# Kernel tuning notes

Measured on AMD Instinct MI355X. Metric: run time of the kernel, lower is better.

The kernel has to match this reference:

```python
import jax, jax.numpy as jnp
import numpy as np

T, D, N, K, H, F = 2048, 4096, 32, 8, 128, 14336
THETA = 500000.0
EPS = 1e-5


def setup_inputs() -> dict:
    key = jax.random.key(0)
    ks = jax.random.split(key, 10)
    s = 0.02  # weight init scale
    return {
        "x": jax.random.normal(ks[0], (T, D), jnp.float32),
        "positions": jnp.arange(T, dtype=jnp.int32),
        "ln1_scale": jnp.ones((D,), jnp.float32),
        "w_q": jax.random.normal(ks[1], (D, N, H), jnp.float32) * s,
        "w_k": jax.random.normal(ks[2], (D, K, H), jnp.float32) * s,
        "w_v": jax.random.normal(ks[3], (D, K, H), jnp.float32) * s,
        "w_o": jax.random.normal(ks[4], (N, H, D), jnp.float32) * s,
        "ln2_scale": jnp.ones((D,), jnp.float32),
        "w_gate": jax.random.normal(ks[5], (D, F), jnp.float32) * s,
        "w_up": jax.random.normal(ks[6], (D, F), jnp.float32) * s,
        "w_down": jax.random.normal(ks[7], (F, D), jnp.float32) * s,
    }


def _rms_norm(x, scale):
    var = jnp.mean(jnp.square(x), axis=-1, keepdims=True)
    return x * jax.lax.rsqrt(var + EPS) * scale


def _apply_rope(x, pos):
    # x: [T, heads, H]; Llama rotate-half RoPE
    half = H // 2
    inv_freq = 1.0 / (THETA ** (jnp.arange(half, dtype=jnp.float32) / half))
    ang = pos.astype(jnp.float32)[:, None] * inv_freq[None, :]      # [T, half]
    cos = jnp.cos(ang)[:, None, :]
    sin = jnp.sin(ang)[:, None, :]
    x1, x2 = x[..., :half], x[..., half:]
    return jnp.concatenate([x1 * cos - x2 * sin, x2 * cos + x1 * sin], axis=-1)


def reference(x, positions, ln1_scale, w_q, w_k, w_v, w_o, ln2_scale, w_gate, w_up, w_down):
    # --- input RMSNorm ---
    h = _rms_norm(x, ln1_scale)
    # --- QKV projections + RoPE ---
    q = _apply_rope(jnp.einsum('td,dnh->tnh', h, w_q), positions)   # [T,N,H]
    k = _apply_rope(jnp.einsum('td,dkh->tkh', h, w_k), positions)   # [T,K,H]
    v = jnp.einsum('td,dkh->tkh', h, w_v)                            # [T,K,H]
    # --- GQA causal attention (prefill) ---
    G = N // K
    qg = q.reshape(T, K, G, H)
    scale = 1.0 / jnp.sqrt(jnp.float32(H))
    scores = jnp.einsum('tkgh,skh->kgts', qg, k) * scale             # [K,G,T,T]
    causal = positions[:, None] >= positions[None, :]                # [T,T]
    scores = jnp.where(causal[None, None], scores, jnp.finfo(scores.dtype).min)
    probs = jax.nn.softmax(scores, axis=-1)
    attn = jnp.einsum('kgts,skh->tkgh', probs, v).reshape(T, N, H)
    attn_out = jnp.einsum('tnh,nhd->td', attn, w_o)
    # --- residual ---
    residual = attn_out + x
    # --- post-attn RMSNorm + SwiGLU MLP ---
    h2 = _rms_norm(residual, ln2_scale)
    gate = jax.nn.silu(h2 @ w_gate)
    up = h2 @ w_up
    out = (gate * up) @ w_down
    return residual + out
```

## Files before the change

### kernel.cpp

```cpp
#include <hip/hip_runtime.h>

typedef __attribute__((ext_vector_type(8))) short bf16x8;
typedef __attribute__((ext_vector_type(4))) float f32x4;

constexpr int T = 2048;
constexpr int D = 4096;
constexpr int NQ = 32;
constexpr int NKV = 8;
constexpr int H = 128;
constexpr int F = 14336;
constexpr int NQKV = (NQ + 2 * NKV) * H;
constexpr int VOFF = (NQ + NKV) * H;

__device__ inline unsigned short f2bf(float f) {
  unsigned u = __float_as_uint(f);
  return (unsigned short)((u + 0x7FFFu + ((u >> 16) & 1u)) >> 16);
}

__device__ inline void gload_lds16(const void* g, void* l) {
  __builtin_amdgcn_global_load_lds((const __attribute__((address_space(1))) void*)g,
                                   (__attribute__((address_space(3))) void*)l, 16, 0, 0);
}

#define MFMA16(a, b, c) __builtin_amdgcn_mfma_f32_16x16x32_bf16(a, b, c, 0, 0, 0)

template <int MODE>
__global__ __launch_bounds__(256) void transpose_bf16(const float* __restrict__ in,
                                                      unsigned short* __restrict__ out,
                                                      int K, int N) {
  __shared__ float tile[64 * 65];
  const int kb = blockIdx.x * 64;
  const int nb = blockIdx.y * 64;
  const int tid = threadIdx.x;
  const int r = tid >> 2;
  const int c4 = tid & 3;
#pragma unroll
  for (int i = 0; i < 4; ++i) {
    float4 v = *(const float4*)(in + (size_t)(kb + r) * N + nb + c4 * 16 + i * 4);
    *(float4*)&tile[r * 65 + c4 * 16 + i * 4] = v;
  }
  __syncthreads();
  const int n = tid >> 2;
  const int kq = tid & 3;
  int nsrc = nb + n;
  int prow = (MODE == 0) ? nsrc : ((nsrc >> 4) * 32 + (nsrc & 15) + (MODE == 2 ? 16 : 0));
#pragma unroll
  for (int half = 0; half < 2; ++half) {
    ushort4 o0, o1;
    int k0 = kq * 16 + half * 8;
    o0.x = f2bf(tile[(k0 + 0) * 65 + n]);
    o0.y = f2bf(tile[(k0 + 1) * 65 + n]);
    o0.z = f2bf(tile[(k0 + 2) * 65 + n]);
    o0.w = f2bf(tile[(k0 + 3) * 65 + n]);
    o1.x = f2bf(tile[(k0 + 4) * 65 + n]);
    o1.y = f2bf(tile[(k0 + 5) * 65 + n]);
    o1.z = f2bf(tile[(k0 + 6) * 65 + n]);
    o1.w = f2bf(tile[(k0 + 7) * 65 + n]);
    unsigned short* op = out + (size_t)prow * K + kb + k0;
    *(ushort4*)(op + 0) = o0;
    *(ushort4*)(op + 4) = o1;
  }
}

__global__ __launch_bounds__(256) void rmsnorm_kernel(
    const float* __restrict__ in, const float* __restrict__ scale,
    unsigned short* __restrict__ out) {
  int row = blockIdx.x;
  const float4* xr = (const float4*)(in + (size_t)row * D);
  const float4* sr = (const float4*)scale;
  float4 vals[4];
  float ss = 0.f;
#pragma unroll
  for (int i = 0; i < 4; ++i) {
    float4 v = xr[threadIdx.x + i * 256];
    vals[i] = v;
    ss += v.x * v.x + v.y * v.y + v.z * v.z + v.w * v.w;
  }
#pragma unroll
  for (int off = 32; off; off >>= 1) ss += __shfl_xor(ss, off, 64);
  __shared__ float wsum[4];
  if ((threadIdx.x & 63) == 0) wsum[threadIdx.x >> 6] = ss;
  __syncthreads();
  float r = rsqrtf((wsum[0] + wsum[1] + wsum[2] + wsum[3]) * (1.f / D) + 1e-5f);
#pragma unroll
  for (int i = 0; i < 4; ++i) {
    int vi = threadIdx.x + i * 256;
    float4 v = vals[i];
    float4 s = sr[vi];
    ushort4 o;
    o.x = f2bf(v.x * r * s.x);
    o.y = f2bf(v.y * r * s.y);
    o.z = f2bf(v.z * r * s.z);
    o.w = f2bf(v.w * r * s.w);
    *(ushort4*)(out + (size_t)row * D + (size_t)vi * 4) = o;
  }
}

__global__ __launch_bounds__(256) void add3_kernel(const float* __restrict__ a,
                                                   const float* __restrict__ b,
                                                   const float* __restrict__ c,
                                                   float* __restrict__ o) {
  int i = blockIdx.x * 256 + threadIdx.x;
  float4 va = ((const float4*)a)[i];
  float4 vb = ((const float4*)b)[i];
  float4 vc = ((const float4*)c)[i];
  float4 vo;
  vo.x = va.x + vb.x + vc.x;
  vo.y = va.y + vb.y + vc.y;
  vo.z = va.z + vb.z + vc.z;
  vo.w = va.w + vb.w + vc.w;
  ((float4*)o)[i] = vo;
}

__global__ __launch_bounds__(256) void rope_table(const int* __restrict__ pos,
                                                  float* __restrict__ ctab,
                                                  float* __restrict__ stab) {
  int idx = blockIdx.x * 256 + threadIdx.x;
  int t = idx >> 6, i = idx & 63;
  float inv = exp2f(-(float)i * (log2f(500000.0f) / 64.0f));
  float ang = (float)pos[t] * inv;
  ctab[idx] = cosf(ang);
  stab[idx] = sinf(ang);
}

__global__ __launch_bounds__(256) void rope_bf16(const float* __restrict__ x,
                                                 const float* __restrict__ ctab,
                                                 const float* __restrict__ stab,
                                                 unsigned short* __restrict__ out,
                                                 int nheads, int row_stride, float scale) {
  int idx = blockIdx.x * 256 + threadIdx.x;
  int i = idx & 63;
  int tn = idx >> 6;
  int t = tn / nheads;
  int n = tn - t * nheads;
  float c = ctab[t * 64 + i], s = stab[t * 64 + i];
  const float* p = x + (size_t)t * row_stride + n * H;
  float x1 = p[i], x2 = p[i + 64];
  unsigned short* o = out + (size_t)tn * H;
  o[i] = f2bf((x1 * c - x2 * s) * scale);
  o[i + 64] = f2bf((x2 * c + x1 * s) * scale);
}

template <int EP>
__global__ __launch_bounds__(256) void gemm_bf(
    const unsigned short* __restrict__ A, const unsigned short* __restrict__ Bt0,
    float* __restrict__ outF, unsigned short* __restrict__ outB, int Kd, int Nd) {
  __shared__ unsigned short lA[128 * 32];
  __shared__ unsigned short lB0[128 * 32];

  const int tid = threadIdx.x;
  const int m0 = blockIdx.x * 128;
  const int n0 = blockIdx.y * 128;
  const int lane = tid & 63;
  const int wv = tid >> 6;

  f32x4 acc[4][4];
#pragma unroll
  for (int i = 0; i < 4; ++i)
#pragma unroll
    for (int j = 0; j < 4; ++j) acc[i][j] = (f32x4){0.f, 0.f, 0.f, 0.f};

  const int wr = (wv >> 1) * 64;
  const int wc = (wv & 1) * 64;
  const int k8 = (lane >> 4) * 8;
  const int rl = lane & 15;
  const int sidx0 = wv * 512 + lane * 8;

  for (int k0 = 0; k0 < Kd; k0 += 32) {
    __syncthreads();
#pragma unroll
    for (int it = 0; it < 2; ++it) {
      int idx = sidx0 + it * 2048;
      int row = idx >> 5, kk = idx & 31;
      int base = wv * 512 + it * 2048;
      gload_lds16(A + (size_t)(m0 + row) * Kd + k0 + kk, &lA[base]);
      gload_lds16(Bt0 + (size_t)(n0 + row) * Kd + k0 + kk, &lB0[base]);
    }
    asm volatile("s_waitcnt vmcnt(0)" ::: "memory");
    __syncthreads();

    bf16x8 af[4], bfr[4];
#pragma unroll
    for (int i = 0; i < 4; ++i)
      af[i] = *(const bf16x8*)&lA[(wr + i * 16 + rl) * 32 + k8];
#pragma unroll
    for (int j = 0; j < 4; ++j)
      bfr[j] = *(const bf16x8*)&lB0[(wc + j * 16 + rl) * 32 + k8];
#pragma unroll
    for (int i = 0; i < 4; ++i)
#pragma unroll
      for (int j = 0; j < 4; ++j)
        acc[i][j] = MFMA16(af[i], bfr[j], acc[i][j]);
  }

  const int rb = (lane >> 4) * 4;
#pragma unroll
  for (int i = 0; i < 4; ++i)
#pragma unroll
    for (int j = 0; j < 4; ++j) {
      int col = n0 + wc + j * 16 + rl;
      if (EP == 4 && n0 >= VOFF) {
        int row0 = m0 + wr + i * 16 + rb;
        ushort4 o;
        o.x = f2bf(acc[i][j][0]);
        o.y = f2bf(acc[i][j][1]);
        o.z = f2bf(acc[i][j][2]);
        o.w = f2bf(acc[i][j][3]);
        *(ushort4*)&outB[(size_t)(col - VOFF) * T + row0] = o;
      } else {
#pragma unroll
        for (int jj = 0; jj < 4; ++jj) {
          int row = m0 + wr + i * 16 + rb + jj;
          outF[(size_t)row * Nd + col] = acc[i][j][jj];
        }
      }
    }
}

template <int EP>
__global__ __launch_bounds__(512, 2) void gemm256(
    const unsigned short* __restrict__ A, const unsigned short* __restrict__ Bt,
    float* __restrict__ outF, float* __restrict__ outF2,
    unsigned short* __restrict__ outB, int Kd, int Nd, int Klen) {
  __shared__ unsigned short lds[65536];
  const int tid = threadIdx.x, lane = tid & 63, wv = tid >> 6;
  const int wm = wv >> 2, wn = wv & 3;
  const int rl = lane & 15, g = lane >> 4;
  const int kz = blockIdx.z;
  int raw = blockIdx.x + blockIdx.y * gridDim.x;
  int cpx = (gridDim.x * gridDim.y) >> 3;
  int sid = (raw & 7) * cpx + (raw >> 3);
  int brow = sid % gridDim.x;
  int bcol = sid / gridDim.x;
  const int m0 = brow * 256, n0 = bcol * 256;

  const int l8 = lane >> 3;
  const int scol = ((lane & 7) ^ l8) * 8;
  const int xr = (rl & 7) << 4;
  const int pc0 = (g * 16) ^ xr;
  const int pc1 = (64 + g * 16) ^ xr;

  const char* ldsc = (const char*)lds;
  const unsigned short* gA = A + (size_t)(m0 + wv * 8 + l8) * Kd + kz * Klen + scol;
  const unsigned short* gB = Bt + (size_t)(n0 + wv * 8 + l8) * Kd + kz * Klen + scol;

  f32x4 acc[8][4];
#pragma unroll
  for (int i = 0; i < 8; ++i)
#pragma unroll
    for (int j = 0; j < 4; ++j) acc[i][j] = (f32x4){0.f, 0.f, 0.f, 0.f};

  const int NT = Klen >> 6;

#define STAGE_AL(kt, l)                                                      \
  gload_lds16(gA + (size_t)(kt) * 64 + (size_t)(l) * 64 * Kd,                \
              (void*)&lds[((kt) & 1) * 32768 + (l) * 4096 + wv * 512]);
#define STAGE_BL(kt, l)                                                      \
  gload_lds16(gB + (size_t)(kt) * 64 + (size_t)(l) * 64 * Kd,                \
              (void*)&lds[((kt) & 1) * 32768 + 16384 + (l) * 4096 + wv * 512]);
#define SBAR()                        \
  __builtin_amdgcn_sched_barrier(0);  \
  __builtin_amdgcn_s_barrier();

  STAGE_AL(0, 0); STAGE_AL(0, 1); STAGE_AL(0, 2); STAGE_AL(0, 3);
  STAGE_BL(0, 0); STAGE_BL(0, 1); STAGE_BL(0, 2); STAGE_BL(0, 3);
  STAGE_AL(1, 0); STAGE_AL(1, 1); STAGE_AL(1, 2); STAGE_AL(1, 3);
  STAGE_BL(1, 0); STAGE_BL(1, 1); STAGE_BL(1, 2); STAGE_BL(1, 3);
  asm volatile("s_waitcnt vmcnt(8)" ::: "memory");
  SBAR();

  const int bhalf = (wn >> 1) * 16384;
  const int brl = (wn & 1) * 64;

  for (int kt = 0; kt < NT; ++kt) {
    const int b = kt & 1;
    const char* aB = ldsc + b * 65536 + wm * 16384;
    const char* bB = ldsc + b * 65536 + 32768 + bhalf;
    const bool pre = (kt + 2 < NT);
    bf16x8 aLo[4][2], aHi[4][2], bLo[2][2], bHi[2][2];
#pragma unroll
    for (int mf = 0; mf < 4; ++mf) {
      aLo[mf][0] = *(const bf16x8*)(aB + (mf * 16 + rl) * 128 + pc0);
      aLo[mf][1] = *(const bf16x8*)(aB + (mf * 16 + rl) * 128 + pc1);
    }
#pragma unroll
    for (int nf = 0; nf < 2; ++nf) {
      bLo[nf][0] = *(const bf16x8*)(bB + (brl + nf * 16 + rl) * 128 + pc0);
      bLo[nf][1] = *(const bf16x8*)(bB + (brl + nf * 16 + rl) * 128 + pc1);
    }
    SBAR();
    __builtin_amdgcn_s_setprio(1);
#pragma unroll
    for (int mf = 0; mf < 4; ++mf)
#pragma unroll
      for (int nf = 0; nf < 2; ++nf) {
        acc[mf][nf] = MFMA16(aLo[mf][0], bLo[nf][0], acc[mf][nf]);
        acc[mf][nf] = MFMA16(aLo[mf][1], bLo[nf][1], acc[mf][nf]);
      }
    __builtin_amdgcn_s_setprio(0);
    SBAR();
#pragma unroll
    for (int nf = 0; nf < 2; ++nf) {
      bHi[nf][0] = *(const bf16x8*)(bB + (brl + (nf + 2) * 16 + rl) * 128 + pc0);
      bHi[nf][1] = *(const bf16x8*)(bB + (brl + (nf + 2) * 16 + rl) * 128 + pc1);
    }
    if (pre) { STAGE_AL(kt + 2, 0); STAGE_AL(kt + 2, 2); }
    SBAR();
    __builtin_amdgcn_s_setprio(1);
#pragma unroll
    for (int mf = 0; mf < 4; ++mf)
#pragma unroll
      for (int nf = 0; nf < 2; ++nf) {
        acc[mf][nf + 2] = MFMA16(aLo[mf][0], bHi[nf][0], acc[mf][nf + 2]);
        acc[mf][nf + 2] = MFMA16(aLo[mf][1], bHi[nf][1], acc[mf][nf + 2]);
      }
    __builtin_amdgcn_s_setprio(0);
    SBAR();
#pragma unroll
    for (int mf = 0; mf < 4; ++mf) {
      aHi[mf][0] = *(const bf16x8*)(aB + ((mf + 4) * 16 + rl) * 128 + pc0);
      aHi[mf][1] = *(const bf16x8*)(aB + ((mf + 4) * 16 + rl) * 128 + pc1);
    }
    if (pre) { STAGE_BL(kt + 2, 0); STAGE_BL(kt + 2, 1); }
    SBAR();
    __builtin_amdgcn_s_setprio(1);
#pragma unroll
    for (int mf = 0; mf < 4; ++mf)
#pragma unroll
      for (int nf = 0; nf < 2; ++nf) {
        acc[mf + 4][nf + 2] = MFMA16(aHi[mf][0], bHi[nf][0], acc[mf + 4][nf + 2]);
        acc[mf + 4][nf + 2] = MFMA16(aHi[mf][1], bHi[nf][1], acc[mf + 4][nf + 2]);
      }
    __builtin_amdgcn_s_setprio(0);
    SBAR();
    if (pre) {
      STAGE_BL(kt + 2, 2); STAGE_BL(kt + 2, 3);
      STAGE_AL(kt + 2, 1); STAGE_AL(kt + 2, 3);
    }
    __builtin_amdgcn_s_setprio(1);
#pragma unroll
    for (int mf = 0; mf < 4; ++mf)
#pragma unroll
      for (int nf = 0; nf < 2; ++nf) {
        acc[mf + 4][nf] = MFMA16(aHi[mf][0], bLo[nf][0], acc[mf + 4][nf]);
        acc[mf + 4][nf] = MFMA16(aHi[mf][1], bLo[nf][1], acc[mf + 4][nf]);
      }
    __builtin_amdgcn_s_setprio(0);
    if (pre) {
      asm volatile("s_waitcnt vmcnt(8)" ::: "memory");
    } else if (kt + 1 < NT) {
      asm volatile("s_waitcnt vmcnt(0)" ::: "memory");
    }
    SBAR();
  }

  const int g4 = g * 4;
  if constexpr (EP == 5) {
    const int acolBase = ((n0 + wn * 64) >> 1) + rl;
#pragma unroll
    for (int mf = 0; mf < 8; ++mf)
#pragma unroll
      for (int p = 0; p < 2; ++p) {
        int acol = acolBase + p * 16;
#pragma unroll
        for (int jj = 0; jj < 4; ++jj) {
          int row = m0 + wm * 128 + mf * 16 + g4 + jj;
          float gg = acc[mf][2 * p][jj];
          float uu = acc[mf][2 * p + 1][jj];
          outB[(size_t)row * F + acol] = f2bf(gg / (1.f + __expf(-gg)) * uu);
        }
      }
  } else {
    float* dst = kz ? outF2 : outF;
#pragma unroll
    for (int mf = 0; mf < 8; ++mf)
#pragma unroll
      for (int q = 0; q < 4; ++q) {
        int col = n0 + wn * 64 + q * 16 + rl;
#pragma unroll
        for (int jj = 0; jj < 4; ++jj) {
          int row = m0 + wm * 128 + mf * 16 + g4 + jj;
          dst[(size_t)row * Nd + col] = acc[mf][q][jj];
        }
      }
  }
#undef STAGE_AL
#undef STAGE_BL
#undef SBAR
}

constexpr int KLD = 136;
constexpr int VLD = 72;
constexpr int PLD = 72;

__global__ __launch_bounds__(256) void flash_attn(
    const unsigned short* __restrict__ qbf, const unsigned short* __restrict__ kbf,
    const unsigned short* __restrict__ vtbf, unsigned short* __restrict__ out) {
  __shared__ unsigned short K_lds[64 * KLD];
  __shared__ unsigned short Vt_lds[H * VLD];
  __shared__ unsigned short P_lds[4 * 16 * PLD];

  const int tid = threadIdx.x;
  const int lane = tid & 63;
  const int wave = tid >> 6;
  const int qb = blockIdx.x;
  const int n = blockIdx.y;
  const int kvh = n >> 2;
  const int g = lane >> 4;
  const int rl = lane & 15;
  const int qrow = qb * 64 + wave * 16;

  bf16x8 qfrag[4];
  {
    const unsigned short* qp = qbf + ((size_t)(qrow + rl) * NQ + n) * H + g * 8;
#pragma unroll
    for (int ks = 0; ks < 4; ++ks) qfrag[ks] = *(const bf16x8*)(qp + ks * 32);
  }

  f32x4 oacc[8];
#pragma unroll
  for (int ob = 0; ob < 8; ++ob) oacc[ob] = (f32x4){0.f, 0.f, 0.f, 0.f};
  float mrun[4] = {-1e30f, -1e30f, -1e30f, -1e30f};
  float lrun[4] = {0.f, 0.f, 0.f, 0.f};

  const int krow = tid >> 2, kseg = (tid & 3) * 32;
  const int vh = tid >> 1, vseg = (tid & 1) * 32;

  for (int kt = 0; kt <= qb; ++kt) {
    const int kbase = kt * 64;
    __syncthreads();
    {
      const unsigned short* kp = kbf + ((size_t)(kbase + krow) * NKV + kvh) * H + kseg;
#pragma unroll
      for (int i = 0; i < 4; ++i)
        *(bf16x8*)&K_lds[krow * KLD + kseg + i * 8] = *(const bf16x8*)(kp + i * 8);
      const unsigned short* vp = vtbf + (size_t)(kvh * H + vh) * T + kbase + vseg;
#pragma unroll
      for (int i = 0; i < 4; ++i)
        *(bf16x8*)&Vt_lds[vh * VLD + vseg + i * 8] = *(const bf16x8*)(vp + i * 8);
    }
    __syncthreads();

    f32x4 sacc[4];
#pragma unroll
    for (int cb = 0; cb < 4; ++cb) sacc[cb] = (f32x4){0.f, 0.f, 0.f, 0.f};
#pragma unroll
    for (int cb = 0; cb < 4; ++cb)
#pragma unroll
      for (int ks = 0; ks < 4; ++ks) {
        bf16x8 kf = *(const bf16x8*)&K_lds[(cb * 16 + rl) * KLD + ks * 32 + g * 8];
        sacc[cb] = MFMA16(qfrag[ks], kf, sacc[cb]);
      }

    if (kt == qb) {
#pragma unroll
      for (int cb = 0; cb < 4; ++cb) {
        int kvg = cb * 16 + rl;
#pragma unroll
        for (int r = 0; r < 4; ++r) {
          int qrel = wave * 16 + g * 4 + r;
          if (kvg > qrel) sacc[cb][r] = -1e30f;
        }
      }
    }

    float mx[4], sm[4], corr[4];
#pragma unroll
    for (int r = 0; r < 4; ++r) {
      float m0 = fmaxf(fmaxf(sacc[0][r], sacc[1][r]), fmaxf(sacc[2][r], sacc[3][r]));
#pragma unroll
      for (int off = 1; off < 16; off <<= 1) m0 = fmaxf(m0, __shfl_xor(m0, off, 64));
      float nm = fmaxf(mrun[r], m0);
      corr[r] = __expf(mrun[r] - nm);
      mrun[r] = nm;
      mx[r] = nm;
    }
#pragma unroll
    for (int cb = 0; cb < 4; ++cb)
#pragma unroll
      for (int r = 0; r < 4; ++r) sacc[cb][r] = __expf(sacc[cb][r] - mx[r]);
#pragma unroll
    for (int r = 0; r < 4; ++r) {
      float s0 = sacc[0][r] + sacc[1][r] + sacc[2][r] + sacc[3][r];
#pragma unroll
      for (int off = 1; off < 16; off <<= 1) s0 += __shfl_xor(s0, off, 64);
      sm[r] = s0;
      lrun[r] = lrun[r] * corr[r] + sm[r];
    }
#pragma unroll
    for (int ob = 0; ob < 8; ++ob)
#pragma unroll
      for (int r = 0; r < 4; ++r) oacc[ob][r] *= corr[r];

#pragma unroll
    for (int cb = 0; cb < 4; ++cb)
#pragma unroll
      for (int r = 0; r < 4; ++r)
        P_lds[(wave * 16 + g * 4 + r) * PLD + cb * 16 + rl] = f2bf(sacc[cb][r]);

    bf16x8 pa[2];
#pragma unroll
    for (int ks = 0; ks < 2; ++ks)
      pa[ks] = *(const bf16x8*)&P_lds[(wave * 16 + rl) * PLD + ks * 32 + g * 8];

#pragma unroll
    for (int ob = 0; ob < 8; ++ob)
#pragma unroll
      for (int ks = 0; ks < 2; ++ks) {
        bf16x8 vf = *(const bf16x8*)&Vt_lds[(ob * 16 + rl) * VLD + ks * 32 + g * 8];
        oacc[ob] = MFMA16(pa[ks], vf, oacc[ob]);
      }
  }

  float inv[4];
#pragma unroll
  for (int r = 0; r < 4; ++r) inv[r] = 1.f / lrun[r];
#pragma unroll
  for (int ob = 0; ob < 8; ++ob)
#pragma unroll
    for (int r = 0; r < 4; ++r) {
      int t = qrow + g * 4 + r;
      out[((size_t)t * NQ + n) * H + ob * 16 + rl] = f2bf(oacc[ob][r] * inv[r]);
    }
}

extern "C" void kernel_launch(void* const* d_in, const int* in_sizes, int n_in,
                              void* d_out, int out_size, void* d_ws, size_t ws_size,
                              hipStream_t stream) {
  (void)in_sizes; (void)n_in; (void)out_size; (void)ws_size;
  const float* x = (const float*)d_in[0];
  const int* positions = (const int*)d_in[1];
  const float* ln1 = (const float*)d_in[2];
  const float* w_q = (const float*)d_in[3];
  const float* w_k = (const float*)d_in[4];
  const float* w_v = (const float*)d_in[5];
  const float* w_o = (const float*)d_in[6];
  const float* ln2 = (const float*)d_in[7];
  const float* w_gate = (const float*)d_in[8];
  const float* w_up = (const float*)d_in[9];
  const float* w_down = (const float*)d_in[10];
  float* out = (float*)d_out;

  char* ws = (char*)d_ws;
  size_t off = 0;
  auto alloc = [&](size_t bytes) {
    char* p = ws + off;
    off += (bytes + 255) & ~(size_t)255;
    return p;
  };
  unsigned short* h_bf = (unsigned short*)alloc((size_t)T * D * 2);
  unsigned short* h2_bf = (unsigned short*)alloc((size_t)T * D * 2);
  unsigned short* attn_bf = (unsigned short*)alloc((size_t)T * NQ * H * 2);
  unsigned short* act_bf = (unsigned short*)alloc((size_t)T * F * 2);
  float* qkvf = (float*)alloc((size_t)T * NQKV * 4);
  float* resid = (float*)alloc((size_t)T * D * 4);
  float* ctab = (float*)alloc((size_t)T * 64 * 4);
  float* stab = (float*)alloc((size_t)T * 64 * 4);
  unsigned short* qbf = (unsigned short*)alloc((size_t)T * NQ * H * 2);
  unsigned short* kbf = (unsigned short*)alloc((size_t)T * NKV * H * 2);
  unsigned short* vtbf = (unsigned short*)alloc((size_t)NKV * H * T * 2);
  unsigned short* wqkvt = (unsigned short*)alloc((size_t)NQKV * D * 2);
  unsigned short* wot = (unsigned short*)alloc((size_t)D * NQ * H * 2);
  unsigned short* wgut = (unsigned short*)alloc((size_t)2 * F * D * 2);
  unsigned short* wdt = (unsigned short*)alloc((size_t)D * F * 2);
  float* part0 = qkvf;
  float* part1 = (float*)wqkvt;

  transpose_bf16<0><<<dim3(D / 64, (NQ * H) / 64), 256, 0, stream>>>(w_q, wqkvt, D, NQ * H);
  transpose_bf16<0><<<dim3(D / 64, (NKV * H) / 64), 256, 0, stream>>>(
      w_k, wqkvt + (size_t)NQ * H * D, D, NKV * H);
  transpose_bf16<0><<<dim3(D / 64, (NKV * H) / 64), 256, 0, stream>>>(
      w_v, wqkvt + (size_t)VOFF * D, D, NKV * H);
  transpose_bf16<0><<<dim3((NQ * H) / 64, D / 64), 256, 0, stream>>>(w_o, wot, NQ * H, D);
  transpose_bf16<1><<<dim3(D / 64, F / 64), 256, 0, stream>>>(w_gate, wgut, D, F);
  transpose_bf16<2><<<dim3(D / 64, F / 64), 256, 0, stream>>>(w_up, wgut, D, F);
  transpose_bf16<0><<<dim3(F / 64, D / 64), 256, 0, stream>>>(w_down, wdt, F, D);

  rmsnorm_kernel<<<T, 256, 0, stream>>>(x, ln1, h_bf);
  rope_table<<<(T * 64) / 256, 256, 0, stream>>>(positions, ctab, stab);
  gemm_bf<4><<<dim3(T / 128, NQKV / 128), 256, 0, stream>>>(
      h_bf, wqkvt, qkvf, vtbf, D, NQKV);
  rope_bf16<<<(T * NQ * 64) / 256, 256, 0, stream>>>(qkvf, ctab, stab, qbf, NQ, NQKV,
                                                     0.08838834764831845f);
  rope_bf16<<<(T * NKV * 64) / 256, 256, 0, stream>>>(qkvf + NQ * H, ctab, stab, kbf,
                                                      NKV, NQKV, 1.0f);
  flash_attn<<<dim3(T / 64, NQ), 256, 0, stream>>>(qbf, kbf, vtbf, attn_bf);
  gemm256<0><<<dim3(T / 256, D / 256, 2), 512, 0, stream>>>(
      attn_bf, wot, part0, part1, nullptr, NQ * H, D, NQ * H / 2);
  add3_kernel<<<(T * D / 4) / 256, 256, 0, stream>>>(part0, part1, x, resid);
  rmsnorm_kernel<<<T, 256, 0, stream>>>(resid, ln2, h2_bf);
  gemm256<5><<<dim3(T / 256, (2 * F) / 256), 512, 0, stream>>>(
      h2_bf, wgut, nullptr, nullptr, act_bf, D, 2 * F, D);
  gemm256<0><<<dim3(T / 256, D / 256, 2), 512, 0, stream>>>(
      act_bf, wdt, part0, part1, nullptr, F, D, F / 2);
  add3_kernel<<<(T * D / 4) / 256, 256, 0, stream>>>(part0, part1, resid, out);
}
```

Measured before the change: 1.401 ms.

## Fuse residual add into RMSNorm, share KV tiles across GQA heads, prefetch B fragments

Three separate changes land together. First, the split-K partial sum plus residual add is fused into the second RMSNorm, which removes one full read and write pass over the residual. Second, flash attention now runs 512 threads per block covering all four query heads of a KV group over 32 query rows, so each K/V tile is loaded once per group instead of once per query head. Third, the 256-tile GEMM main loop reorders its B-tile staging and waits so that the next iteration's B low fragments are read from LDS early and carried in registers. The GEMM change raises register pressure and shifts the vmcnt wait points, and the attention change alters grid size and occupancy.

Result: no change. 1.378 ms (-1.6%).

```diff
diff --git a/kernel.cpp b/kernel.cpp
--- a/kernel.cpp
+++ b/kernel.cpp
@@ -86,6 +86,51 @@
   for (int i = 0; i < 4; ++i) {
     int vi = threadIdx.x + i * 256;
     float4 v = vals[i];
+    float4 s = sr[vi];
+    ushort4 o;
+    o.x = f2bf(v.x * r * s.x);
+    o.y = f2bf(v.y * r * s.y);
+    o.z = f2bf(v.z * r * s.z);
+    o.w = f2bf(v.w * r * s.w);
+    *(ushort4*)(out + (size_t)row * D + (size_t)vi * 4) = o;
+  }
+}
+
+__global__ __launch_bounds__(256) void rmsnorm_add3(
+    const float* __restrict__ a, const float* __restrict__ b,
+    const float* __restrict__ c, const float* __restrict__ scale,
+    float* __restrict__ residOut, unsigned short* __restrict__ out) {
+  int row = blockIdx.x;
+  const float4* ar = (const float4*)(a + (size_t)row * D);
+  const float4* br = (const float4*)(b + (size_t)row * D);
+  const float4* cr = (const float4*)(c + (size_t)row * D);
+  const float4* sr = (const float4*)scale;
+  float4* rr = (float4*)(residOut + (size_t)row * D);
+  float4 vals[4];
+  float ss = 0.f;
+#pragma unroll
+  for (int i = 0; i < 4; ++i) {
+    int vi = threadIdx.x + i * 256;
+    float4 va = ar[vi], vb = br[vi], vc = cr[vi];
+    float4 v;
+    v.x = va.x + vb.x + vc.x;
+    v.y = va.y + vb.y + vc.y;
+    v.z = va.z + vb.z + vc.z;
+    v.w = va.w + vb.w + vc.w;
+    vals[i] = v;
+    ss += v.x * v.x + v.y * v.y + v.z * v.z + v.w * v.w;
+  }
+#pragma unroll
+  for (int off = 32; off; off >>= 1) ss += __shfl_xor(ss, off, 64);
+  __shared__ float wsum[4];
+  if ((threadIdx.x & 63) == 0) wsum[threadIdx.x >> 6] = ss;
+  __syncthreads();
+  float r = rsqrtf((wsum[0] + wsum[1] + wsum[2] + wsum[3]) * (1.f / D) + 1e-5f);
+#pragma unroll
+  for (int i = 0; i < 4; ++i) {
+    int vi = threadIdx.x + i * 256;
+    float4 v = vals[i];
+    rr[vi] = v;
     float4 s = sr[vi];
     ushort4 o;
     o.x = f2bf(v.x * r * s.x);
@@ -272,30 +317,36 @@
   const int bhalf = (wn >> 1) * 16384;
   const int brl = (wn & 1) * 64;
 
+  bf16x8 bLoC[2][2];
+  {
+    const char* bB0 = ldsc + 32768 + bhalf;
+#pragma unroll
+    for (int nf = 0; nf < 2; ++nf) {
+      bLoC[nf][0] = *(const bf16x8*)(bB0 + (brl + nf * 16 + rl) * 128 + pc0);
+      bLoC[nf][1] = *(const bf16x8*)(bB0 + (brl + nf * 16 + rl) * 128 + pc1);
+    }
+  }
+
   for (int kt = 0; kt < NT; ++kt) {
     const int b = kt & 1;
     const char* aB = ldsc + b * 65536 + wm * 16384;
     const char* bB = ldsc + b * 65536 + 32768 + bhalf;
+    const char* bBn = ldsc + (b ^ 1) * 65536 + 32768 + bhalf;
     const bool pre = (kt + 2 < NT);
-    bf16x8 aLo[4][2], aHi[4][2], bLo[2][2], bHi[2][2];
+    bf16x8 aLo[4][2], aHi[4][2], bHi[2][2], bLoN[2][2];
 #pragma unroll
     for (int mf = 0; mf < 4; ++mf) {
       aLo[mf][0] = *(const bf16x8*)(aB + (mf * 16 + rl) * 128 + pc0);
       aLo[mf][1] = *(const bf16x8*)(aB + (mf * 16 + rl) * 128 + pc1);
     }
-#pragma unroll
-    for (int nf = 0; nf < 2; ++nf) {
-      bLo[nf][0] = *(const bf16x8*)(bB + (brl + nf * 16 + rl) * 128 + pc0);
-      bLo[nf][1] = *(const bf16x8*)(bB + (brl + nf * 16 + rl) * 128 + pc1);
-    }
     SBAR();
     __builtin_amdgcn_s_setprio(1);
 #pragma unroll
     for (int mf = 0; mf < 4; ++mf)
 #pragma unroll
       for (int nf = 0; nf < 2; ++nf) {
-        acc[mf][nf] = MFMA16(aLo[mf][0], bLo[nf][0], acc[mf][nf]);
-        acc[mf][nf] = MFMA16(aLo[mf][1], bLo[nf][1], acc[mf][nf]);
+        acc[mf][nf] = MFMA16(aLo[mf][0], bLoC[nf][0], acc[mf][nf]);
+        acc[mf][nf] = MFMA16(aLo[mf][1], bLoC[nf][1], acc[mf][nf]);
       }
     __builtin_amdgcn_s_setprio(0);
     SBAR();
@@ -321,7 +372,13 @@
       aHi[mf][0] = *(const bf16x8*)(aB + ((mf + 4) * 16 + rl) * 128 + pc0);
       aHi[mf][1] = *(const bf16x8*)(aB + ((mf + 4) * 16 + rl) * 128 + pc1);
     }
-    if (pre) { STAGE_BL(kt + 2, 0); STAGE_BL(kt + 2, 1); }
+    if (pre) {
+      STAGE_BL(kt + 2, 0); STAGE_BL(kt + 2, 1);
+      STAGE_BL(kt + 2, 2); STAGE_BL(kt + 2, 3);
+      asm volatile("s_waitcnt vmcnt(6)" ::: "memory");
+    } else {
+      asm volatile("s_waitcnt vmcnt(0)" ::: "memory");
+    }
     SBAR();
     __builtin_amdgcn_s_setprio(1);
 #pragma unroll
@@ -333,25 +390,32 @@
       }
     __builtin_amdgcn_s_setprio(0);
     SBAR();
-    if (pre) {
-      STAGE_BL(kt + 2, 2); STAGE_BL(kt + 2, 3);
-      STAGE_AL(kt + 2, 1); STAGE_AL(kt + 2, 3);
-    }
+    if (pre) { STAGE_AL(kt + 2, 1); STAGE_AL(kt + 2, 3); }
+    if (kt + 1 < NT) {
+#pragma unroll
+      for (int nf = 0; nf < 2; ++nf) {
+        bLoN[nf][0] = *(const bf16x8*)(bBn + (brl + nf * 16 + rl) * 128 + pc0);
+        bLoN[nf][1] = *(const bf16x8*)(bBn + (brl + nf * 16 + rl) * 128 + pc1);
+      }
+    }
+    SBAR();
     __builtin_amdgcn_s_setprio(1);
 #pragma unroll
     for (int mf = 0; mf < 4; ++mf)
 #pragma unroll
       for (int nf = 0; nf < 2; ++nf) {
-        acc[mf + 4][nf] = MFMA16(aHi[mf][0], bLo[nf][0], acc[mf + 4][nf]);
-        acc[mf + 4][nf] = MFMA16(aHi[mf][1], bLo[nf][1], acc[mf + 4][nf]);
+        acc[mf + 4][nf] = MFMA16(aHi[mf][0], bLoC[nf][0], acc[mf + 4][nf]);
+        acc[mf + 4][nf] = MFMA16(aHi[mf][1], bLoC[nf][1], acc[mf + 4][nf]);
       }
     __builtin_amdgcn_s_setprio(0);
-    if (pre) {
-      asm volatile("s_waitcnt vmcnt(8)" ::: "memory");
-    } else if (kt + 1 < NT) {
-      asm volatile("s_waitcnt vmcnt(0)" ::: "memory");
-    }
-    SBAR();
+    SBAR();
+    if (kt + 1 < NT) {
+#pragma unroll
+      for (int nf = 0; nf < 2; ++nf) {
+        bLoC[nf][0] = bLoN[nf][0];
+        bLoC[nf][1] = bLoN[nf][1];
+      }
+    }
   }
 
   const int g4 = g * 4;
@@ -393,22 +457,23 @@
 constexpr int VLD = 72;
 constexpr int PLD = 72;
 
-__global__ __launch_bounds__(256) void flash_attn(
+__global__ __launch_bounds__(512) void flash_attn(
     const unsigned short* __restrict__ qbf, const unsigned short* __restrict__ kbf,
     const unsigned short* __restrict__ vtbf, unsigned short* __restrict__ out) {
   __shared__ unsigned short K_lds[64 * KLD];
   __shared__ unsigned short Vt_lds[H * VLD];
-  __shared__ unsigned short P_lds[4 * 16 * PLD];
+  __shared__ unsigned short P_lds[8 * 16 * PLD];
 
   const int tid = threadIdx.x;
   const int lane = tid & 63;
-  const int wave = tid >> 6;
+  const int wv = tid >> 6;
   const int qb = blockIdx.x;
-  const int n = blockIdx.y;
-  const int kvh = n >> 2;
+  const int kvh = blockIdx.y;
+  const int qh = wv & 3, rh = wv >> 2;
+  const int n = kvh * 4 + qh;
   const int g = lane >> 4;
   const int rl = lane & 15;
-  const int qrow = qb * 64 + wave * 16;
+  const int qrow = qb * 32 + rh * 16;
 
   bf16x8 qfrag[4];
   {
@@ -423,21 +488,20 @@
   float mrun[4] = {-1e30f, -1e30f, -1e30f, -1e30f};
   float lrun[4] = {0.f, 0.f, 0.f, 0.f};
 
-  const int krow = tid >> 2, kseg = (tid & 3) * 32;
-  const int vh = tid >> 1, vseg = (tid & 1) * 32;
-
-  for (int kt = 0; kt <= qb; ++kt) {
+  const int krow = tid >> 3, kseg = (tid & 7) * 16;
+  const int vh = tid >> 2, vseg = (tid & 3) * 16;
+
+  const int ktmax = (qb * 32 + 31) >> 6;
+  for (int kt = 0; kt <= ktmax; ++kt) {
     const int kbase = kt * 64;
     __syncthreads();
     {
       const unsigned short* kp = kbf + ((size_t)(kbase + krow) * NKV + kvh) * H + kseg;
-#pragma unroll
-      for (int i = 0; i < 4; ++i)
-        *(bf16x8*)&K_lds[krow * KLD + kseg + i * 8] = *(const bf16x8*)(kp + i * 8);
+      *(bf16x8*)&K_lds[krow * KLD + kseg] = *(const bf16x8*)kp;
+      *(bf16x8*)&K_lds[krow * KLD + kseg + 8] = *(const bf16x8*)(kp + 8);
       const unsigned short* vp = vtbf + (size_t)(kvh * H + vh) * T + kbase + vseg;
-#pragma unroll
-      for (int i = 0; i < 4; ++i)
-        *(bf16x8*)&Vt_lds[vh * VLD + vseg + i * 8] = *(const bf16x8*)(vp + i * 8);
+      *(bf16x8*)&Vt_lds[vh * VLD + vseg] = *(const bf16x8*)vp;
+      *(bf16x8*)&Vt_lds[vh * VLD + vseg + 8] = *(const bf16x8*)(vp + 8);
     }
     __syncthreads();
 
@@ -452,14 +516,13 @@
         sacc[cb] = MFMA16(qfrag[ks], kf, sacc[cb]);
       }
 
-    if (kt == qb) {
+    if (kt == ktmax) {
 #pragma unroll
       for (int cb = 0; cb < 4; ++cb) {
-        int kvg = cb * 16 + rl;
+        int kv_abs = kbase + cb * 16 + rl;
 #pragma unroll
         for (int r = 0; r < 4; ++r) {
-          int qrel = wave * 16 + g * 4 + r;
-          if (kvg > qrel) sacc[cb][r] = -1e30f;
+          if (kv_abs > qrow + g * 4 + r) sacc[cb][r] = -1e30f;
         }
       }
     }
@@ -496,12 +559,12 @@
     for (int cb = 0; cb < 4; ++cb)
 #pragma unroll
       for (int r = 0; r < 4; ++r)
-        P_lds[(wave * 16 + g * 4 + r) * PLD + cb * 16 + rl] = f2bf(sacc[cb][r]);
+        P_lds[(wv * 16 + g * 4 + r) * PLD + cb * 16 + rl] = f2bf(sacc[cb][r]);
 
     bf16x8 pa[2];
 #pragma unroll
     for (int ks = 0; ks < 2; ++ks)
-      pa[ks] = *(const bf16x8*)&P_lds[(wave * 16 + rl) * PLD + ks * 32 + g * 8];
+      pa[ks] = *(const bf16x8*)&P_lds[(wv * 16 + rl) * PLD + ks * 32 + g * 8];
 
 #pragma unroll
     for (int ob = 0; ob < 8; ++ob)
@@ -584,11 +647,10 @@
                                                      0.08838834764831845f);
   rope_bf16<<<(T * NKV * 64) / 256, 256, 0, stream>>>(qkvf + NQ * H, ctab, stab, kbf,
                                                       NKV, NQKV, 1.0f);
-  flash_attn<<<dim3(T / 64, NQ), 256, 0, stream>>>(qbf, kbf, vtbf, attn_bf);
+  flash_attn<<<dim3(T / 32, NKV), 512, 0, stream>>>(qbf, kbf, vtbf, attn_bf);
   gemm256<0><<<dim3(T / 256, D / 256, 2), 512, 0, stream>>>(
       attn_bf, wot, part0, part1, nullptr, NQ * H, D, NQ * H / 2);
-  add3_kernel<<<(T * D / 4) / 256, 256, 0, stream>>>(part0, part1, x, resid);
-  rmsnorm_kernel<<<T, 256, 0, stream>>>(resid, ln2, h2_bf);
+  rmsnorm_add3<<<T, 256, 0, stream>>>(part0, part1, x, ln2, resid, h2_bf);
   gemm256<5><<<dim3(T / 256, (2 * F) / 256), 512, 0, stream>>>(
       h2_bf, wgut, nullptr, nullptr, act_bf, D, 2 * F, D);
   gemm256<0><<<dim3(T / 256, D / 256, 2), 512, 0, stream>>>(
```
